# Kernel optimization log

Hardware: AMD Instinct MI355X
Metric: run time of the kernel (lower is better)

The kernel has to match this reference:

```python
import jax, jax.numpy as jnp
import numpy as np

N = 50000      # nodes
E = 800000     # edges
IN, HID, OUT = 256, 512, 256
EPS = 1e-5     # BatchNorm eps


def setup_inputs() -> dict:
    key = jax.random.key(0)
    ks = jax.random.split(key, 12)
    x = jax.random.normal(ks[0], (N, IN), jnp.float32)
    edge_index = jax.random.randint(ks[1], (2, E), 0, N, jnp.int32)

    def lin(k, fi, fo):
        return jax.random.normal(k, (fi, fo), jnp.float32) / np.sqrt(fi).astype(np.float32)

    return {
        "x": x,
        "edge_index": edge_index,
        "W1": lin(ks[2], IN, HID),  "b1": jnp.zeros((HID,), jnp.float32),
        "g1": jnp.ones((HID,), jnp.float32), "be1": jnp.zeros((HID,), jnp.float32),
        "W2": lin(ks[3], HID, HID), "b2": jnp.zeros((HID,), jnp.float32),
        "g2": jnp.ones((HID,), jnp.float32), "be2": jnp.zeros((HID,), jnp.float32),
        "W3": lin(ks[4], HID, OUT), "b3": jnp.zeros((OUT,), jnp.float32),
    }


def _gcn_conv(x, W, b, src, dst, dinv):
    # PyG GCNConv: D^{-1/2}(A+I)D^{-1/2} X W + b, edge weights = 1
    h = x @ W                                   # [N, F_out] dense transform
    norm = (dinv[src] * dinv[dst])[:, None]     # [E, 1]
    agg = jax.ops.segment_sum(h[src] * norm, dst, num_segments=N)
    agg = agg + h * (dinv * dinv)[:, None]      # self-loop contribution
    return agg + b


def _bn(h, g, b):
    # BatchNorm1d, training-mode batch statistics over node dim
    m = h.mean(axis=0)
    v = h.var(axis=0)
    return (h - m) * jax.lax.rsqrt(v + EPS) * g + b


def reference(x, edge_index, W1, b1, g1, be1, W2, b2, g2, be2, W3, b3):
    src, dst = edge_index[0], edge_index[1]
    # symmetric normalization degrees (incl. self loop)
    deg = jax.ops.segment_sum(jnp.ones((E,), jnp.float32), dst, num_segments=N) + 1.0
    dinv = jax.lax.rsqrt(deg)

    residual = x  # in_feats == out_feats -> nn.Identity
    h = jax.nn.relu(_bn(_gcn_conv(x, W1, b1, src, dst, dinv), g1, be1))
    h = jax.nn.relu(_bn(_gcn_conv(h, W2, b2, src, dst, dinv), g2, be2))
    h = _gcn_conv(h, W3, b3, src, dst, dinv)
    return h + residual
```

## Files before the change

kernel.cpp:

```cpp
#include <hip/hip_runtime.h>
#include <hip/hip_bf16.h>

#define NN 50000
#define NE 800000

typedef unsigned short u16;
typedef unsigned int   u32;

typedef __attribute__((ext_vector_type(8))) __bf16 bf16x8;
typedef __attribute__((ext_vector_type(4))) float  f32x4;

__device__ __forceinline__ float bf2f(u16 x) {
    u32 u = ((u32)x) << 16;
    return __builtin_bit_cast(float, u);
}
__device__ __forceinline__ u16 f2bf(float f) {
    u32 u = __builtin_bit_cast(u32, f);
    u32 r = (u + 0x7FFFu + ((u >> 16) & 1u)) >> 16;
    return (u16)r;
}
__device__ __forceinline__ float bflo(u32 w) { return __builtin_bit_cast(float, w << 16); }
__device__ __forceinline__ float bfhi(u32 w) { return __builtin_bit_cast(float, w & 0xffff0000u); }


__global__ __launch_bounds__(256) void count_k(const int* __restrict__ dst, int* __restrict__ deg, int E) {
    int e = blockIdx.x * 256 + threadIdx.x;
    if (e < E) atomicAdd(&deg[dst[e]], 1);
}

__global__ __launch_bounds__(256) void dinv_k(const int* __restrict__ deg, float* __restrict__ dinv, int n) {
    int i = blockIdx.x * 256 + threadIdx.x;
    if (i < n) dinv[i] = rsqrtf((float)deg[i] + 1.0f);
}

__global__ __launch_bounds__(256) void scan1_k(const int* __restrict__ deg, int* __restrict__ bsum, int n) {
    __shared__ int sd[256];
    int i = blockIdx.x * 256 + threadIdx.x;
    sd[threadIdx.x] = (i < n) ? deg[i] : 0;
    __syncthreads();
    for (int s = 128; s > 0; s >>= 1) {
        if (threadIdx.x < s) sd[threadIdx.x] += sd[threadIdx.x + s];
        __syncthreads();
    }
    if (threadIdx.x == 0) bsum[blockIdx.x] = sd[0];
}

__global__ __launch_bounds__(256) void scan2_k(int* __restrict__ bsum, int nb) {
    __shared__ int sd[256];
    int t = threadIdx.x;
    int v = (t < nb) ? bsum[t] : 0;
    sd[t] = v;
    __syncthreads();
    for (int off = 1; off < 256; off <<= 1) {
        int tv = (t >= off) ? sd[t - off] : 0;
        __syncthreads();
        sd[t] += tv;
        __syncthreads();
    }
    if (t < nb) bsum[t] = sd[t] - v;
}

__global__ __launch_bounds__(256) void scan3_k(const int* __restrict__ deg, const int* __restrict__ bofs,
                                               int* __restrict__ rs, int* __restrict__ cur, int n) {
    __shared__ int sd[256];
    int t = threadIdx.x;
    int i = blockIdx.x * 256 + t;
    int v = (i < n) ? deg[i] : 0;
    sd[t] = v;
    __syncthreads();
    for (int off = 1; off < 256; off <<= 1) {
        int tv = (t >= off) ? sd[t - off] : 0;
        __syncthreads();
        sd[t] += tv;
        __syncthreads();
    }
    int excl = sd[t] - v + bofs[blockIdx.x];
    if (i < n) { rs[i] = excl; cur[i] = excl; }
}

__global__ __launch_bounds__(256) void fill_k(const int* __restrict__ src, const int* __restrict__ dst,
                                              int* __restrict__ cur, int* __restrict__ csr, int E) {
    int e = blockIdx.x * 256 + threadIdx.x;
    if (e < E) {
        int d = dst[e];
        int pos = atomicAdd(&cur[d], 1);
        csr[pos] = src[e];
    }
}


__global__ __launch_bounds__(256) void cast_k(const float* __restrict__ X, u16* __restrict__ Y, int total) {
    int idx = (blockIdx.x * 256 + threadIdx.x) * 8;
    if (idx >= total) return;
    float4 a = *(const float4*)(X + idx);
    float4 b = *(const float4*)(X + idx + 4);
    uint4 o;
    o.x = (u32)f2bf(a.x) | ((u32)f2bf(a.y) << 16);
    o.y = (u32)f2bf(a.z) | ((u32)f2bf(a.w) << 16);
    o.z = (u32)f2bf(b.x) | ((u32)f2bf(b.y) << 16);
    o.w = (u32)f2bf(b.z) | ((u32)f2bf(b.w) << 16);
    *(uint4*)(Y + idx) = o;
}


__global__ __launch_bounds__(256) void transpose_k(const float* __restrict__ W, u16* __restrict__ Wt, int K, int F) {
    __shared__ float t[32][33];
    int k0 = blockIdx.x * 32, f0 = blockIdx.y * 32;
    int tx = threadIdx.x & 31, ty = threadIdx.x >> 5;
    for (int r = ty; r < 32; r += 8) t[r][tx] = W[(size_t)(k0 + r) * F + f0 + tx];
    __syncthreads();
    for (int r = ty; r < 32; r += 8) Wt[(size_t)(f0 + r) * K + k0 + tx] = f2bf(t[tx][r]);
}


template <int F, int MODE>
__global__ __launch_bounds__(256) void aggu_k(const u16* __restrict__ X, u16* __restrict__ Y,
                                              float* __restrict__ Yf,
                                              const float* __restrict__ dinv, const int* __restrict__ rs,
                                              const int* __restrict__ dg, const int* __restrict__ csr,
                                              const float* __restrict__ scale, const float* __restrict__ shift,
                                              const float* __restrict__ b3, const float* __restrict__ xres) {
    constexpr int FB = F / 64;
    const int i = blockIdx.x;
    const int tid = threadIdx.x;
    const int sl = tid >> 6;
    const int lane = tid & 63;
    const int start = rs[i], cnt = dg[i];
    const float di = dinv[i];

    __shared__ int   s_idx[64];
    __shared__ float s_w[64];
    __shared__ float red[4][F];

    float sc[FB], sh[FB];
    if constexpr (MODE == 1) {
        #pragma unroll
        for (int k = 0; k < FB; k++) {
            sc[k] = scale[lane * FB + k];
            sh[k] = shift[lane * FB + k];
        }
    }

    float acc[FB];
    #pragma unroll
    for (int k = 0; k < FB; k++) acc[k] = 0.f;

    auto gadd = [&](int row, float wgt) {
        float v[FB];
        if constexpr (FB == 4) {
            uint2 p = *(const uint2*)(X + (size_t)row * F + lane * 4);
            v[0] = bflo(p.x); v[1] = bfhi(p.x);
            v[2] = bflo(p.y); v[3] = bfhi(p.y);
        } else {
            uint4 p = *(const uint4*)(X + (size_t)row * F + lane * 8);
            v[0] = bflo(p.x); v[1] = bfhi(p.x);
            v[2] = bflo(p.y); v[3] = bfhi(p.y);
            v[4] = bflo(p.z); v[5] = bfhi(p.z);
            v[6] = bflo(p.w); v[7] = bfhi(p.w);
        }
        #pragma unroll
        for (int k = 0; k < FB; k++) {
            if constexpr (MODE == 1) v[k] = fmaxf(fmaf(v[k], sc[k], sh[k]), 0.f);
            acc[k] = fmaf(v[k], wgt, acc[k]);
        }
    };

    if (sl == 0) gadd(i, di);

    for (int base = 0; base < cnt; base += 64) {
        const int m = min(64, cnt - base);
        __syncthreads();
        if (tid < m) {
            int s = csr[start + base + tid];
            s_idx[tid] = s;
            s_w[tid] = dinv[s];
        }
        __syncthreads();
        #pragma unroll 2
        for (int jj = sl; jj < m; jj += 4)
            gadd(s_idx[jj], s_w[jj]);
    }

    #pragma unroll
    for (int k = 0; k < FB; k++) red[sl][lane * FB + k] = acc[k];
    __syncthreads();

    if constexpr (MODE == 2) {
        const int f = tid;
        float v = red[0][f] + red[1][f] + red[2][f] + red[3][f];
        Yf[(size_t)i * 256 + f] = v * di + b3[f] + xres[(size_t)i * 256 + f];
    } else {
        if (tid < F / 2) {
            const int f0 = tid * 2;
            float v0 = (red[0][f0] + red[1][f0] + red[2][f0] + red[3][f0]) * di;
            float v1 = (red[0][f0 + 1] + red[1][f0 + 1] + red[2][f0 + 1] + red[3][f0 + 1]) * di;
            *(u32*)(Y + (size_t)i * F + f0) = (u32)f2bf(v0) | ((u32)f2bf(v1) << 16);
        }
    }
}


template <bool STATS, bool BIAS>
__global__ __launch_bounds__(256) void gemm_k(const u16* __restrict__ A, const u16* __restrict__ Wt,
                                              const float* __restrict__ bias, u16* __restrict__ C,
                                              float* __restrict__ colsum, float* __restrict__ colsq,
                                              int M, int K, int F) {
    __shared__ u16 As[128 * 40];
    __shared__ u16 Bs[128 * 40];
    const int m0 = blockIdx.x * 128, f0 = blockIdx.y * 128;
    const int tid = threadIdx.x;
    const int lane = tid & 63, wave = tid >> 6;
    const int waveM = (wave >> 1) * 64, waveN = (wave & 1) * 64;
    const int lrow = tid >> 2, lch = tid & 3;

    f32x4 acc[4][4];
    const f32x4 fz = {0.f, 0.f, 0.f, 0.f};
    #pragma unroll
    for (int i = 0; i < 4; i++)
        #pragma unroll
        for (int j = 0; j < 4; j++) acc[i][j] = fz;

    const int rA0 = m0 + lrow, rA1 = m0 + 64 + lrow;
    const u16* pA0 = A + (size_t)rA0 * K + lch * 8;
    const u16* pA1 = A + (size_t)rA1 * K + lch * 8;
    const u16* pB0 = Wt + (size_t)(f0 + lrow) * K + lch * 8;
    const u16* pB1 = Wt + (size_t)(f0 + 64 + lrow) * K + lch * 8;
    u16* qA0 = &As[lrow * 40 + lch * 8];
    u16* qA1 = &As[(64 + lrow) * 40 + lch * 8];
    u16* qB0 = &Bs[lrow * 40 + lch * 8];
    u16* qB1 = &Bs[(64 + lrow) * 40 + lch * 8];
    const uint4 z4 = {0u, 0u, 0u, 0u};

    const int fm = lane & 15, fq = lane >> 4;

    for (int k0 = 0; k0 < K; k0 += 32) {
        uint4 a0 = (rA0 < M) ? *(const uint4*)(pA0 + k0) : z4;
        uint4 a1 = (rA1 < M) ? *(const uint4*)(pA1 + k0) : z4;
        uint4 b0 = *(const uint4*)(pB0 + k0);
        uint4 b1 = *(const uint4*)(pB1 + k0);
        __syncthreads();
        *(uint4*)qA0 = a0;
        *(uint4*)qA1 = a1;
        *(uint4*)qB0 = b0;
        *(uint4*)qB1 = b1;
        __syncthreads();
        bf16x8 af[4], bfr[4];
        #pragma unroll
        for (int i = 0; i < 4; i++)
            af[i] = *(const bf16x8*)&As[(waveM + i * 16 + fm) * 40 + fq * 8];
        #pragma unroll
        for (int j = 0; j < 4; j++)
            bfr[j] = *(const bf16x8*)&Bs[(waveN + j * 16 + fm) * 40 + fq * 8];
        #pragma unroll
        for (int i = 0; i < 4; i++)
            #pragma unroll
            for (int j = 0; j < 4; j++)
                acc[i][j] = __builtin_amdgcn_mfma_f32_16x16x32_bf16(af[i], bfr[j], acc[i][j], 0, 0, 0);
    }

    #pragma unroll
    for (int j = 0; j < 4; j++) {
        const int col = f0 + waveN + j * 16 + fm;
        const float bcol = BIAS ? bias[col] : 0.f;
        float s = 0.f, s2 = 0.f;
        #pragma unroll
        for (int i = 0; i < 4; i++) {
            const int rb = m0 + waveM + i * 16 + fq * 4;
            #pragma unroll
            for (int r = 0; r < 4; r++) {
                const int row = rb + r;
                if (row < M) {
                    float v = acc[i][j][r] + bcol;
                    C[(size_t)row * F + col] = f2bf(v);
                    if (STATS) { s += v; s2 += v * v; }
                }
            }
        }
        if (STATS) {
            s += __shfl_xor(s, 16);
            s += __shfl_xor(s, 32);
            s2 += __shfl_xor(s2, 16);
            s2 += __shfl_xor(s2, 32);
            if (fq == 0) {
                atomicAdd(&colsum[col], s);
                atomicAdd(&colsq[col], s2);
            }
        }
    }
}


__global__ __launch_bounds__(256) void bnfin_k(const float* __restrict__ sum, const float* __restrict__ sq,
                                               const float* __restrict__ g, const float* __restrict__ be,
                                               float* __restrict__ scale, float* __restrict__ shift,
                                               int F, float invN) {
    int f = blockIdx.x * 256 + threadIdx.x;
    if (f < F) {
        float m = sum[f] * invN;
        float v = sq[f] * invN - m * m;
        float s = rsqrtf(v + 1e-5f) * g[f];
        scale[f] = s;
        shift[f] = be[f] - m * s;
    }
}

__global__ __launch_bounds__(256) void bnrelu_k(u16* __restrict__ H, const float* __restrict__ scale,
                                                const float* __restrict__ shift, int total, int F) {
    int idx = blockIdx.x * 256 + threadIdx.x;
    int base = idx * 8;
    if (base >= total) return;
    uint4 p = *(const uint4*)(H + base);
    int col = base & (F - 1);
    u32 w[4] = {p.x, p.y, p.z, p.w};
    u32 o[4];
    #pragma unroll
    for (int q = 0; q < 4; q++) {
        float x0 = fmaxf(bflo(w[q]) * scale[col + 2 * q] + shift[col + 2 * q], 0.f);
        float x1 = fmaxf(bfhi(w[q]) * scale[col + 2 * q + 1] + shift[col + 2 * q + 1], 0.f);
        o[q] = ((u32)f2bf(x1) << 16) | (u32)f2bf(x0);
    }
    uint4 po = {o[0], o[1], o[2], o[3]};
    *(uint4*)(H + base) = po;
}


extern "C" void kernel_launch(void* const* d_in, const int* in_sizes, int n_in,
                              void* d_out, int out_size, void* d_ws, size_t ws_size,
                              hipStream_t stream) {
    const float* x   = (const float*)d_in[0];
    const int*   ei  = (const int*)d_in[1];
    const float* W1  = (const float*)d_in[2];
    const float* b1  = (const float*)d_in[3];
    const float* pg1 = (const float*)d_in[4];
    const float* pbe1= (const float*)d_in[5];
    const float* W2  = (const float*)d_in[6];
    const float* b2  = (const float*)d_in[7];
    const float* pg2 = (const float*)d_in[8];
    const float* pbe2= (const float*)d_in[9];
    const float* W3  = (const float*)d_in[10];
    const float* b3  = (const float*)d_in[11];
    float* out = (float*)d_out;

    char* ws = (char*)d_ws;
    size_t off = 0;
    auto alloc = [&](size_t bytes) -> char* {
        char* p = ws + off;
        off += (bytes + 255) & ~(size_t)255;
        return p;
    };
    float* dinv  = (float*)alloc(NN * 4);
    int*   deg   = (int*)alloc(NN * 4);
    int*   rs    = (int*)alloc(NN * 4);
    int*   cur   = (int*)alloc(NN * 4);
    int*   bsum  = (int*)alloc(256 * 4);
    int*   csr   = (int*)alloc(NE * 4);
    float* stats = (float*)alloc(4 * 512 * 4);
    float* cs1 = stats, *cq1 = stats + 512, *cs2 = stats + 1024, *cq2 = stats + 1536;
    float* scale1 = (float*)alloc(512 * 4);
    float* shift1 = (float*)alloc(512 * 4);
    float* scale2 = (float*)alloc(512 * 4);
    float* shift2 = (float*)alloc(512 * 4);
    u16*   W1t   = (u16*)alloc((size_t)512 * 256 * 2);
    u16*   W2t   = (u16*)alloc((size_t)512 * 512 * 2);
    u16*   W3t   = (u16*)alloc((size_t)256 * 512 * 2);
    u16*   HB    = (u16*)alloc((size_t)NN * 512 * 2);
    u16*   G3    = (u16*)alloc((size_t)NN * 256 * 2);

    u16* XB = G3;
    u16* A1 = (u16*)d_out;
    u16* A2 = (u16*)d_out;

    const int* srcp = ei;
    const int* dstp = ei + NE;

    hipMemsetAsync(deg, 0, NN * 4, stream);
    hipMemsetAsync(stats, 0, 4 * 512 * 4, stream);

    const int nbN = (NN + 255) / 256;
    count_k<<<(NE + 255) / 256, 256, 0, stream>>>(dstp, deg, NE);
    dinv_k<<<nbN, 256, 0, stream>>>(deg, dinv, NN);
    scan1_k<<<nbN, 256, 0, stream>>>(deg, bsum, NN);
    scan2_k<<<1, 256, 0, stream>>>(bsum, nbN);
    scan3_k<<<nbN, 256, 0, stream>>>(deg, bsum, rs, cur, NN);
    fill_k<<<(NE + 255) / 256, 256, 0, stream>>>(srcp, dstp, cur, csr, NE);

    transpose_k<<<dim3(256 / 32, 512 / 32), 256, 0, stream>>>(W1, W1t, 256, 512);
    transpose_k<<<dim3(512 / 32, 512 / 32), 256, 0, stream>>>(W2, W2t, 512, 512);
    transpose_k<<<dim3(512 / 32, 256 / 32), 256, 0, stream>>>(W3, W3t, 512, 256);

    cast_k<<<NN * 256 / 8 / 256, 256, 0, stream>>>(x, XB, NN * 256);

    const int MT = (NN + 127) / 128;

    aggu_k<256, 0><<<NN, 256, 0, stream>>>(XB, A1, nullptr, dinv, rs, deg, csr,
                                           nullptr, nullptr, nullptr, nullptr);
    gemm_k<true, true><<<dim3(MT, 4), 256, 0, stream>>>(A1, W1t, b1, HB, cs1, cq1, NN, 256, 512);
    bnfin_k<<<2, 256, 0, stream>>>(cs1, cq1, pg1, pbe1, scale1, shift1, 512, 1.f / NN);

    aggu_k<512, 1><<<NN, 256, 0, stream>>>(HB, A2, nullptr, dinv, rs, deg, csr,
                                           scale1, shift1, nullptr, nullptr);
    gemm_k<true, true><<<dim3(MT, 4), 256, 0, stream>>>(A2, W2t, b2, HB, cs2, cq2, NN, 512, 512);
    bnfin_k<<<2, 256, 0, stream>>>(cs2, cq2, pg2, pbe2, scale2, shift2, 512, 1.f / NN);
    bnrelu_k<<<NN * 512 / 8 / 256, 256, 0, stream>>>(HB, scale2, shift2, NN * 512, 512);

    gemm_k<false, false><<<dim3(MT, 2), 256, 0, stream>>>(HB, W3t, nullptr, G3, nullptr, nullptr, NN, 512, 256);
    aggu_k<256, 2><<<NN, 256, 0, stream>>>(G3, nullptr, out, dinv, rs, deg, csr,
                                           nullptr, nullptr, b3, x);
}
```

Measured before the change: 712.8 us.

## Store layer-1 activations in FP8 and fuse BN+ReLU into layer-3 GEMM load

```diff
diff --git a/kernel.cpp b/kernel.cpp
--- a/kernel.cpp
+++ b/kernel.cpp
@@ -6,6 +6,7 @@
 
 typedef unsigned short u16;
 typedef unsigned int   u32;
+typedef unsigned char  u8;
 
 typedef __attribute__((ext_vector_type(8))) __bf16 bf16x8;
 typedef __attribute__((ext_vector_type(4))) float  f32x4;
@@ -21,6 +22,20 @@
 }
 __device__ __forceinline__ float bflo(u32 w) { return __builtin_bit_cast(float, w << 16); }
 __device__ __forceinline__ float bfhi(u32 w) { return __builtin_bit_cast(float, w & 0xffff0000u); }
+
+__device__ __forceinline__ u32 bnpack2(u32 w, float sc0, float sc1, float sh0, float sh1) {
+    float x0 = fmaxf(fmaf(bflo(w), sc0, sh0), 0.f);
+    float x1 = fmaxf(fmaf(bfhi(w), sc1, sh1), 0.f);
+    return (u32)f2bf(x0) | ((u32)f2bf(x1) << 16);
+}
+__device__ __forceinline__ uint4 bnpack8(uint4 a, float4 sa, float4 sb, float4 ha, float4 hb) {
+    uint4 o;
+    o.x = bnpack2(a.x, sa.x, sa.y, ha.x, ha.y);
+    o.y = bnpack2(a.y, sa.z, sa.w, ha.z, ha.w);
+    o.z = bnpack2(a.z, sb.x, sb.y, hb.x, hb.y);
+    o.w = bnpack2(a.w, sb.z, sb.w, hb.z, hb.w);
+    return o;
+}
 
 
 __global__ __launch_bounds__(256) void count_k(const int* __restrict__ dst, int* __restrict__ deg, int E) {
@@ -113,8 +128,8 @@
 }
 
 
-template <int F, int MODE>
-__global__ __launch_bounds__(256) void aggu_k(const u16* __restrict__ X, u16* __restrict__ Y,
+template <int F, int MODE, int TBL>
+__global__ __launch_bounds__(256) void aggu_k(const void* __restrict__ Xv, u16* __restrict__ Y,
                                               float* __restrict__ Yf,
                                               const float* __restrict__ dinv, const int* __restrict__ rs,
                                               const int* __restrict__ dg, const int* __restrict__ csr,
@@ -147,11 +162,24 @@
 
     auto gadd = [&](int row, float wgt) {
         float v[FB];
-        if constexpr (FB == 4) {
+        if constexpr (TBL == 1) {
+            const u8* X8 = (const u8*)Xv;
+            uint2 p = *(const uint2*)(X8 + (size_t)row * F + lane * 8);
+            v[0] = __builtin_amdgcn_cvt_f32_fp8(p.x, 0);
+            v[1] = __builtin_amdgcn_cvt_f32_fp8(p.x, 1);
+            v[2] = __builtin_amdgcn_cvt_f32_fp8(p.x, 2);
+            v[3] = __builtin_amdgcn_cvt_f32_fp8(p.x, 3);
+            v[4] = __builtin_amdgcn_cvt_f32_fp8(p.y, 0);
+            v[5] = __builtin_amdgcn_cvt_f32_fp8(p.y, 1);
+            v[6] = __builtin_amdgcn_cvt_f32_fp8(p.y, 2);
+            v[7] = __builtin_amdgcn_cvt_f32_fp8(p.y, 3);
+        } else if constexpr (FB == 4) {
+            const u16* X = (const u16*)Xv;
             uint2 p = *(const uint2*)(X + (size_t)row * F + lane * 4);
             v[0] = bflo(p.x); v[1] = bfhi(p.x);
             v[2] = bflo(p.y); v[3] = bfhi(p.y);
         } else {
+            const u16* X = (const u16*)Xv;
             uint4 p = *(const uint4*)(X + (size_t)row * F + lane * 8);
             v[0] = bflo(p.x); v[1] = bfhi(p.x);
             v[2] = bflo(p.y); v[3] = bfhi(p.y);
@@ -200,10 +228,11 @@
 }
 
 
-template <bool STATS, bool BIAS>
+template <bool STATS, bool BIAS, bool CFP8, bool ABN>
 __global__ __launch_bounds__(256) void gemm_k(const u16* __restrict__ A, const u16* __restrict__ Wt,
-                                              const float* __restrict__ bias, u16* __restrict__ C,
+                                              const float* __restrict__ bias, void* __restrict__ C,
                                               float* __restrict__ colsum, float* __restrict__ colsq,
+                                              const float* __restrict__ ascale, const float* __restrict__ ashift,
                                               int M, int K, int F) {
     __shared__ u16 As[128 * 40];
     __shared__ u16 Bs[128 * 40];
@@ -238,6 +267,14 @@
         uint4 a1 = (rA1 < M) ? *(const uint4*)(pA1 + k0) : z4;
         uint4 b0 = *(const uint4*)(pB0 + k0);
         uint4 b1 = *(const uint4*)(pB1 + k0);
+        if constexpr (ABN) {
+            const float4 sa = *(const float4*)(ascale + k0 + lch * 8);
+            const float4 sb = *(const float4*)(ascale + k0 + lch * 8 + 4);
+            const float4 ha = *(const float4*)(ashift + k0 + lch * 8);
+            const float4 hb = *(const float4*)(ashift + k0 + lch * 8 + 4);
+            a0 = bnpack8(a0, sa, sb, ha, hb);
+            a1 = bnpack8(a1, sa, sb, ha, hb);
+        }
         __syncthreads();
         *(uint4*)qA0 = a0;
         *(uint4*)qA1 = a1;
@@ -271,7 +308,12 @@
                 const int row = rb + r;
                 if (row < M) {
                     float v = acc[i][j][r] + bcol;
-                    C[(size_t)row * F + col] = f2bf(v);
+                    if constexpr (CFP8) {
+                        u32 q = __builtin_amdgcn_cvt_pk_fp8_f32(v, v, 0u, false);
+                        ((u8*)C)[(size_t)row * F + col] = (u8)(q & 0xffu);
+                    } else {
+                        ((u16*)C)[(size_t)row * F + col] = f2bf(v);
+                    }
                     if (STATS) { s += v; s2 += v * v; }
                 }
             }
@@ -302,25 +344,6 @@
         scale[f] = s;
         shift[f] = be[f] - m * s;
     }
-}
-
-__global__ __launch_bounds__(256) void bnrelu_k(u16* __restrict__ H, const float* __restrict__ scale,
-                                                const float* __restrict__ shift, int total, int F) {
-    int idx = blockIdx.x * 256 + threadIdx.x;
-    int base = idx * 8;
-    if (base >= total) return;
-    uint4 p = *(const uint4*)(H + base);
-    int col = base & (F - 1);
-    u32 w[4] = {p.x, p.y, p.z, p.w};
-    u32 o[4];
-    #pragma unroll
-    for (int q = 0; q < 4; q++) {
-        float x0 = fmaxf(bflo(w[q]) * scale[col + 2 * q] + shift[col + 2 * q], 0.f);
-        float x1 = fmaxf(bfhi(w[q]) * scale[col + 2 * q + 1] + shift[col + 2 * q + 1], 0.f);
-        o[q] = ((u32)f2bf(x1) << 16) | (u32)f2bf(x0);
-    }
-    uint4 po = {o[0], o[1], o[2], o[3]};
-    *(uint4*)(H + base) = po;
 }
 
 
@@ -363,12 +386,14 @@
     u16*   W1t   = (u16*)alloc((size_t)512 * 256 * 2);
     u16*   W2t   = (u16*)alloc((size_t)512 * 512 * 2);
     u16*   W3t   = (u16*)alloc((size_t)256 * 512 * 2);
-    u16*   HB    = (u16*)alloc((size_t)NN * 512 * 2);
+    u16*   REG   = (u16*)alloc((size_t)NN * 512 * 2);
     u16*   G3    = (u16*)alloc((size_t)NN * 256 * 2);
 
-    u16* XB = G3;
-    u16* A1 = (u16*)d_out;
-    u16* A2 = (u16*)d_out;
+    u8*  HB1 = (u8*)REG;
+    u16* H2  = REG;
+    u16* XB  = G3;
+    u16* A1  = (u16*)d_out;
+    u16* A2  = (u16*)d_out;
 
     const int* srcp = ei;
     const int* dstp = ei + NE;
@@ -392,18 +417,20 @@
 
     const int MT = (NN + 127) / 128;
 
-    aggu_k<256, 0><<<NN, 256, 0, stream>>>(XB, A1, nullptr, dinv, rs, deg, csr,
-                                           nullptr, nullptr, nullptr, nullptr);
-    gemm_k<true, true><<<dim3(MT, 4), 256, 0, stream>>>(A1, W1t, b1, HB, cs1, cq1, NN, 256, 512);
+    aggu_k<256, 0, 0><<<NN, 256, 0, stream>>>(XB, A1, nullptr, dinv, rs, deg, csr,
+                                              nullptr, nullptr, nullptr, nullptr);
+    gemm_k<true, true, true, false><<<dim3(MT, 4), 256, 0, stream>>>(
+        A1, W1t, b1, HB1, cs1, cq1, nullptr, nullptr, NN, 256, 512);
     bnfin_k<<<2, 256, 0, stream>>>(cs1, cq1, pg1, pbe1, scale1, shift1, 512, 1.f / NN);
 
-    aggu_k<512, 1><<<NN, 256, 0, stream>>>(HB, A2, nullptr, dinv, rs, deg, csr,
-                                           scale1, shift1, nullptr, nullptr);
-    gemm_k<true, true><<<dim3(MT, 4), 256, 0, stream>>>(A2, W2t, b2, HB, cs2, cq2, NN, 512, 512);
+    aggu_k<512, 1, 1><<<NN, 256, 0, stream>>>(HB1, A2, nullptr, dinv, rs, deg, csr,
+                                              scale1, shift1, nullptr, nullptr);
+    gemm_k<true, true, false, false><<<dim3(MT, 4), 256, 0, stream>>>(
+        A2, W2t, b2, H2, cs2, cq2, nullptr, nullptr, NN, 512, 512);
     bnfin_k<<<2, 256, 0, stream>>>(cs2, cq2, pg2, pbe2, scale2, shift2, 512, 1.f / NN);
-    bnrelu_k<<<NN * 512 / 8 / 256, 256, 0, stream>>>(HB, scale2, shift2, NN * 512, 512);
-
-    gemm_k<false, false><<<dim3(MT, 2), 256, 0, stream>>>(HB, W3t, nullptr, G3, nullptr, nullptr, NN, 512, 256);
-    aggu_k<256, 2><<<NN, 256, 0, stream>>>(G3, nullptr, out, dinv, rs, deg, csr,
-                                           nullptr, nullptr, b3, x);
-}
+
+    gemm_k<false, false, false, true><<<dim3(MT, 2), 256, 0, stream>>>(
+        H2, W3t, nullptr, G3, nullptr, nullptr, scale2, shift2, NN, 512, 256);
+    aggu_k<256, 2, 0><<<NN, 256, 0, stream>>>(G3, nullptr, out, dinv, rs, deg, csr,
+                                              nullptr, nullptr, b3, x);
+}
```

New measurement: 726.0 us. Within noise of the previous version (+1.9%).
